# Kernel optimization log

Measured on AMD Instinct MI355X. Metric: run time of the kernel, lower is better.

Reference implementation:

```python
import itertools
import jax, jax.numpy as jnp
import numpy as np

FS = 16000
MAX_TAU = 40
C_SOUND = 343.0
MIC_DISTANCE_FROM_WALL = 0.5
MIN_SPEAKER_HEIGHT = 1.0
MAX_SPEAKER_HEIGHT = 2.0
ROOM = (6.0, 5.0, 3.0)
DENSITY = (0.1, 0.1, 0.1)
N_MICS = 8


def _build_geometry():
    # 8-mic circular array, radius 0.4 m, centered in the room
    ang = np.arange(N_MICS) * 2.0 * np.pi / N_MICS
    receivers = np.stack([3.0 + 0.4 * np.cos(ang),
                          2.5 + 0.4 * np.sin(ang),
                          1.5 * np.ones(N_MICS)], axis=1).astype(np.float32)  # [M,3]
    combinations = np.array(list(itertools.combinations(range(N_MICS), 2)), dtype=np.int32)  # [P,2]
    # candidate grid (same nesting order as the original list comprehension)
    xs = np.arange(MIC_DISTANCE_FROM_WALL, ROOM[0] + DENSITY[0], DENSITY[0], dtype=np.float32)
    ys = np.arange(0.0, ROOM[1] + DENSITY[1], DENSITY[1], dtype=np.float32)
    zs = np.arange(MIN_SPEAKER_HEIGHT, MAX_SPEAKER_HEIGHT + DENSITY[2], DENSITY[2], dtype=np.float32)
    grid_x = np.stack(np.meshgrid(xs, ys, zs, indexing='ij'), axis=-1).reshape(-1, 3)  # [G,3]
    # true TDOA per grid point / pair -> delay index into GCC output of length 2*MAX_TAU+1
    rp = receivers[combinations]                                   # [P,2,3]
    d = np.linalg.norm(grid_x[:, None, None, :] - rp[None], axis=-1)  # [G,P,2]
    tdoa = (d[..., 0] - d[..., 1]) / C_SOUND * FS                  # samples
    tau = np.clip(MAX_TAU + np.round(tdoa), 0, 2 * MAX_TAU).astype(np.int32)  # [G,P]
    rec_centroid = receivers.mean(axis=0)                          # [3]
    return grid_x, tau, combinations, rec_centroid


def setup_inputs() -> dict:
    key = jax.random.key(0)
    signal = jax.random.normal(key, (16, N_MICS, 4096), dtype=jnp.float32)
    grid_x, tau, combinations, rec_centroid = _build_geometry()
    return {
        "signal": signal,
        "grid_x": jnp.asarray(grid_x),
        "tau": jnp.asarray(tau),
        "combinations": jnp.asarray(combinations),
        "rec_centroid": jnp.asarray(rec_centroid),
    }


def reference(signal, grid_x, tau, combinations, rec_centroid):
    B, M, N = signal.shape
    P = combinations.shape[0]
    # GCC-PHAT per mic pair
    pairs = signal[:, combinations, :]                    # [B,P,2,N]
    S = jnp.fft.rfft(pairs, axis=-1)                      # [B,P,2,F]
    X = S[..., 0, :] * jnp.conj(S[..., 1, :])             # cross-spectrum [B,P,F]
    phat = X / (jnp.abs(X) + 1e-12)
    cc = jnp.fft.irfft(phat, n=N, axis=-1)                # [B,P,N]
    # lags -MAX_TAU..MAX_TAU -> length 2*MAX_TAU+1
    cc = jnp.concatenate([cc[..., -MAX_TAU:], cc[..., :MAX_TAU + 1]], axis=-1)  # [B,P,2T+1]
    # gather per grid point / pair (avoids materializing [B,G,P,2T+1])
    gathered = cc[:, jnp.arange(P)[None, :], tau]         # [B,G,P]
    power = gathered.sum(axis=-1)                         # SRP map [B,G]
    idx = jnp.argmax(power, axis=-1)                      # [B]
    x = grid_x[idx]                                       # [B,3]
    return x - rec_centroid
```

## Files before the change

### kernel.cpp

```cpp
#include <hip/hip_runtime.h>

#define N_FFT 4096
#define NH    2048
#define NBINS 2049
#define NLAGS 81
#define MAXTAU 40
#define NSEG  4
#define SEGLEN 512
#define PI_D 3.14159265358979323846

__global__ void table_kernel(double2* __restrict__ tw_fft,
                             double2* __restrict__ tw_post) {
    int idx = blockIdx.x * 256 + (int)threadIdx.x;
    if (idx < 1024) {
        double sv, cv;
        sincos(-(2.0 * PI_D / (double)NH) * (double)idx, &sv, &cv);
        tw_fft[idx] = make_double2(cv, sv);
    } else if (idx < 1024 + NBINS) {
        int k = idx - 1024;
        double sv, cv;
        sincos(-(2.0 * PI_D / (double)N_FFT) * (double)k, &sv, &cv);
        tw_post[k] = make_double2(cv, sv);
    }
}

__global__ __launch_bounds__(1024)
void rfft_kernel(const float* __restrict__ sig,
                 const double2* __restrict__ tw_fft,
                 const double2* __restrict__ tw_post,
                 double* __restrict__ S) {
    int bm  = blockIdx.x;
    int tid = (int)threadIdx.x;

    __shared__ double2 data[NH];

    const float2* sp = (const float2*)(sig + (size_t)bm * N_FFT);
    for (int i = tid; i < NH; i += 1024) {
        float2 v = sp[i];
        int j = (int)(__brev((unsigned)i) >> 21);
        data[j] = make_double2((double)v.x, (double)v.y);
    }
    __syncthreads();

    for (int s = 1; s <= 11; ++s) {
        int half = 1 << (s - 1);
        int t  = tid;
        int g  = t >> (s - 1);
        int j  = t & (half - 1);
        int i0 = (g << s) + j;
        int i1 = i0 + half;
        double2 w = tw_fft[j << (11 - s)];
        double2 u = data[i0];
        double2 v = data[i1];
        double vr = v.x * w.x - v.y * w.y;
        double vi = v.x * w.y + v.y * w.x;
        data[i0] = make_double2(u.x + vr, u.y + vi);
        data[i1] = make_double2(u.x - vr, u.y - vi);
        __syncthreads();
    }

    double* So = S + (size_t)bm * NBINS * 2;
    for (int k = tid; k < NBINS; k += 1024) {
        double2 Zk = data[k & (NH - 1)];
        double2 Zm = data[(NH - k) & (NH - 1)];
        double er = 0.5 * (Zk.x + Zm.x);
        double ei = 0.5 * (Zk.y - Zm.y);
        double dr = Zk.x - Zm.x;
        double di = Zk.y + Zm.y;
        double orr = 0.5 * di;
        double oii = -0.5 * dr;
        double2 w = tw_post[k];
        So[k * 2]     = er + w.x * orr - w.y * oii;
        So[k * 2 + 1] = ei + w.x * oii + w.y * orr;
    }
}

#define NCH 6
#define CHLEN 86
__global__ __launch_bounds__(256)
void phat_cc_part_kernel(const double* __restrict__ S,
                         const int* __restrict__ comb,
                         double* __restrict__ cc_part, int P) {
    int id  = (int)blockIdx.x;
    int seg = id & (NSEG - 1);
    int bp  = id >> 2;
    int b   = bp / P;
    int p   = bp % P;
    int ma = comb[p * 2 + 0];
    int mb = comb[p * 2 + 1];
    const double2* Sa = (const double2*)(S + ((size_t)(b * 8 + ma)) * NBINS * 2);
    const double2* Sb = (const double2*)(S + ((size_t)(b * 8 + mb)) * NBINS * 2);

    int k0 = seg * SEGLEN;
    int k1 = (seg == NSEG - 1) ? NBINS : (k0 + SEGLEN);

    __shared__ double2 phs[SEGLEN + 1];
    __shared__ double partCr[41 * NCH];
    __shared__ double partCi[41 * NCH];

    int tid = (int)threadIdx.x;
    for (int k = k0 + tid; k < k1; k += 256) {
        double2 a = Sa[k];
        double2 c = Sb[k];
        double Xr = a.x * c.x + a.y * c.y;
        double Xi = a.y * c.x - a.x * c.y;
        double mag = sqrt(Xr * Xr + Xi * Xi);
        double w = (k == 0 || k == 2048) ? 1.0 : 2.0;
        double inv = w / (mag + 1e-12);
        phs[k - k0] = make_double2(Xr * inv, Xi * inv);
    }
    __syncthreads();

    if (tid < 41 * NCH) {
        int n = tid % 41;
        int c = tid / 41;
        int kk0 = k0 + c * CHLEN;
        int kk1 = kk0 + CHLEN;
        if (kk1 > k1) kk1 = k1;

        double step = (2.0 * PI_D / (double)N_FFT) * (double)n;
        double sv, cv;
        sincos(step, &sv, &cv);
        double wr = cv, wi = sv;
        sincos(step * (double)kk0, &sv, &cv);
        double rr = cv, ri = sv;

        double Cr = 0.0, Ci = 0.0;
        for (int k = kk0; k < kk1; ++k) {
            double2 ph = phs[k - k0];
            Cr = fma(ph.x, rr, Cr);
            Ci = fma(ph.y, ri, Ci);
            double nr = rr * wr - ri * wi;
            double ni = rr * wi + ri * wr;
            rr = nr; ri = ni;
        }
        partCr[tid] = Cr;
        partCi[tid] = Ci;
    }
    __syncthreads();

    if (tid < 41) {
        double Cr = 0.0, Ci = 0.0;
        #pragma unroll
        for (int c = 0; c < NCH; ++c) {
            Cr += partCr[tid + 41 * c];
            Ci += partCi[tid + 41 * c];
        }
        double* out = cc_part + ((size_t)bp * NSEG + (size_t)seg) * NLAGS;
        out[MAXTAU + tid] = Cr - Ci;
        if (tid > 0) out[MAXTAU - tid] = Cr + Ci;
    }
}

__global__ void cc_reduce_kernel(const double* __restrict__ cc_part,
                                 double* __restrict__ cc, int total) {
    int idx = blockIdx.x * 256 + (int)threadIdx.x;
    if (idx >= total) return;
    int bp  = idx / NLAGS;
    int lag = idx % NLAGS;
    const double* src = cc_part + (size_t)bp * NSEG * NLAGS + lag;
    double v = 0.0;
    #pragma unroll
    for (int s = 0; s < NSEG; ++s) v += src[s * NLAGS];
    cc[idx] = v * (1.0 / (double)N_FFT);
}

__global__ __launch_bounds__(256)
void power_argmax_kernel(const double* __restrict__ cc,
                         const int* __restrict__ tau,
                         int G, int P,
                         double* __restrict__ pval,
                         int* __restrict__ pidx, int nchunks) {
    int b     = (int)blockIdx.y;
    int chunk = (int)blockIdx.x;
    int tid   = (int)threadIdx.x;

    __shared__ double ccs[28 * NLAGS];
    const double2* csrc = (const double2*)(cc + (size_t)b * P * NLAGS);
    double2* cdst = (double2*)ccs;
    for (int i = tid; i < 28 * NLAGS / 2; i += 256) cdst[i] = csrc[i];
    __syncthreads();

    int g = chunk * 256 + tid;
    double v = -1e300;
    int    gi = 0x7fffffff;
    if (g < G) {
        const int4* tp = (const int4*)(tau + (size_t)g * 28);
        v = 0.0;
        #pragma unroll
        for (int q = 0; q < 7; ++q) {
            int4 tv = tp[q];
            v += ccs[(q * 4 + 0) * NLAGS + tv.x];
            v += ccs[(q * 4 + 1) * NLAGS + tv.y];
            v += ccs[(q * 4 + 2) * NLAGS + tv.z];
            v += ccs[(q * 4 + 3) * NLAGS + tv.w];
        }
        gi = g;
    }

    #pragma unroll
    for (int off = 32; off > 0; off >>= 1) {
        double v2 = __shfl_down(v, off);
        int    i2 = __shfl_down(gi, off);
        if (v2 > v || (v2 == v && i2 < gi)) { v = v2; gi = i2; }
    }
    __shared__ double wval[4];
    __shared__ int    widx[4];
    int lane = tid & 63, wv = tid >> 6;
    if (lane == 0) { wval[wv] = v; widx[wv] = gi; }
    __syncthreads();
    if (tid == 0) {
        #pragma unroll
        for (int w = 1; w < 4; ++w) {
            double v2 = wval[w]; int i2 = widx[w];
            if (v2 > v || (v2 == v && i2 < gi)) { v = v2; gi = i2; }
        }
        pval[b * nchunks + chunk] = v;
        pidx[b * nchunks + chunk] = gi;
    }
}

__global__ void finalize_kernel(const double* __restrict__ pval,
                                const int* __restrict__ pidx, int nchunks,
                                const float* __restrict__ grid_x,
                                const float* __restrict__ rec_centroid,
                                float* __restrict__ out) {
    int b = (int)blockIdx.x;
    int l = (int)threadIdx.x;
    double v = -1e300; int gi = 0x7fffffff;
    for (int j = l; j < nchunks; j += 64) {
        double v2 = pval[b * nchunks + j];
        int    i2 = pidx[b * nchunks + j];
        if (v2 > v || (v2 == v && i2 < gi)) { v = v2; gi = i2; }
    }
    #pragma unroll
    for (int off = 32; off > 0; off >>= 1) {
        double v2 = __shfl_down(v, off);
        int    i2 = __shfl_down(gi, off);
        if (v2 > v || (v2 == v && i2 < gi)) { v = v2; gi = i2; }
    }
    if (l == 0) {
        for (int c = 0; c < 3; ++c)
            out[b * 3 + c] = grid_x[(size_t)gi * 3 + c] - rec_centroid[c];
    }
}

extern "C" void kernel_launch(void* const* d_in, const int* in_sizes, int n_in,
                              void* d_out, int out_size, void* d_ws, size_t ws_size,
                              hipStream_t stream) {
    const float* signal       = (const float*)d_in[0];
    const float* grid_x       = (const float*)d_in[1];
    const int*   tau          = (const int*)d_in[2];
    const int*   comb         = (const int*)d_in[3];
    const float* rec_centroid = (const float*)d_in[4];
    float* out = (float*)d_out;

    int G  = in_sizes[1] / 3;
    int P  = in_sizes[3] / 2;
    int BM = in_sizes[0] / N_FFT;
    int B  = BM / 8;
    int BP = B * P;

    double*  S       = (double*)d_ws;
    double*  cc      = S + (size_t)BM * NBINS * 2;
    double*  cc_part = cc + (size_t)BP * NLAGS;
    double2* tw_fft  = (double2*)(cc_part + (size_t)BP * NSEG * NLAGS);
    double2* tw_post = tw_fft + 1024;
    int nchunks = (G + 255) / 256;
    double*  pval = (double*)(tw_post + NBINS);
    int*     pidx = (int*)(pval + (size_t)B * nchunks);

    table_kernel<<<13, 256, 0, stream>>>(tw_fft, tw_post);
    rfft_kernel<<<BM, 1024, 0, stream>>>(signal, tw_fft, tw_post, S);
    phat_cc_part_kernel<<<BP * NSEG, 256, 0, stream>>>(S, comb, cc_part, P);
    cc_reduce_kernel<<<(BP * NLAGS + 255) / 256, 256, 0, stream>>>(cc_part, cc, BP * NLAGS);
    power_argmax_kernel<<<dim3(nchunks, B), 256, 0, stream>>>(cc, tau, G, P, pval, pidx, nchunks);
    finalize_kernel<<<B, 64, 0, stream>>>(pval, pidx, nchunks, grid_x, rec_centroid, out);
}
```

Measured before the change: 109.1 us.

## Fuse cc reduction and finalize into power-argmax, double phat segments

Splits the PHAT/cross-correlation work into 8 segments instead of 4, doubling the number of blocks for more parallelism. The separate cc_reduce kernel is removed: each power_argmax block sums the segment partials itself while loading its shared cc table. The finalize kernel is replaced by a last-block-done ticket scheme using atomics and fences, so the final argmax and output write happen in the last block to finish. Together this removes two kernel launches, at the cost of redundant partial summation in every power block and atomic/fence overhead.

Result: slower. 183.7 us (+68.4%).

```diff
diff --git a/kernel.cpp b/kernel.cpp
--- a/kernel.cpp
+++ b/kernel.cpp
@@ -5,12 +5,13 @@
 #define NBINS 2049
 #define NLAGS 81
 #define MAXTAU 40
-#define NSEG  4
-#define SEGLEN 512
+#define NSEG  8
+#define SEGLEN 256
 #define PI_D 3.14159265358979323846
 
 __global__ void table_kernel(double2* __restrict__ tw_fft,
-                             double2* __restrict__ tw_post) {
+                             double2* __restrict__ tw_post,
+                             int* __restrict__ ticket, int B) {
     int idx = blockIdx.x * 256 + (int)threadIdx.x;
     if (idx < 1024) {
         double sv, cv;
@@ -22,6 +23,7 @@
         sincos(-(2.0 * PI_D / (double)N_FFT) * (double)k, &sv, &cv);
         tw_post[k] = make_double2(cv, sv);
     }
+    if (idx < B) ticket[idx] = 0;
 }
 
 __global__ __launch_bounds__(1024)
@@ -76,14 +78,14 @@
 }
 
 #define NCH 6
-#define CHLEN 86
+#define CHLEN 43
 __global__ __launch_bounds__(256)
 void phat_cc_part_kernel(const double* __restrict__ S,
                          const int* __restrict__ comb,
                          double* __restrict__ cc_part, int P) {
     int id  = (int)blockIdx.x;
     int seg = id & (NSEG - 1);
-    int bp  = id >> 2;
+    int bp  = id >> 3;
     int b   = bp / P;
     int p   = bp % P;
     int ma = comb[p * 2 + 0];
@@ -146,39 +148,36 @@
             Cr += partCr[tid + 41 * c];
             Ci += partCi[tid + 41 * c];
         }
-        double* out = cc_part + ((size_t)bp * NSEG + (size_t)seg) * NLAGS;
-        out[MAXTAU + tid] = Cr - Ci;
-        if (tid > 0) out[MAXTAU - tid] = Cr + Ci;
-    }
-}
-
-__global__ void cc_reduce_kernel(const double* __restrict__ cc_part,
-                                 double* __restrict__ cc, int total) {
-    int idx = blockIdx.x * 256 + (int)threadIdx.x;
-    if (idx >= total) return;
-    int bp  = idx / NLAGS;
-    int lag = idx % NLAGS;
-    const double* src = cc_part + (size_t)bp * NSEG * NLAGS + lag;
-    double v = 0.0;
-    #pragma unroll
-    for (int s = 0; s < NSEG; ++s) v += src[s * NLAGS];
-    cc[idx] = v * (1.0 / (double)N_FFT);
+        double* outp = cc_part + ((size_t)bp * NSEG + (size_t)seg) * NLAGS;
+        outp[MAXTAU + tid] = Cr - Ci;
+        if (tid > 0) outp[MAXTAU - tid] = Cr + Ci;
+    }
 }
 
 __global__ __launch_bounds__(256)
-void power_argmax_kernel(const double* __restrict__ cc,
+void power_argmax_kernel(const double* __restrict__ cc_part,
                          const int* __restrict__ tau,
                          int G, int P,
                          double* __restrict__ pval,
-                         int* __restrict__ pidx, int nchunks) {
+                         int* __restrict__ pidx, int nchunks,
+                         int* __restrict__ ticket,
+                         const float* __restrict__ grid_x,
+                         const float* __restrict__ rec_centroid,
+                         float* __restrict__ out) {
     int b     = (int)blockIdx.y;
     int chunk = (int)blockIdx.x;
     int tid   = (int)threadIdx.x;
 
     __shared__ double ccs[28 * NLAGS];
-    const double2* csrc = (const double2*)(cc + (size_t)b * P * NLAGS);
-    double2* cdst = (double2*)ccs;
-    for (int i = tid; i < 28 * NLAGS / 2; i += 256) cdst[i] = csrc[i];
+    for (int i = tid; i < 28 * NLAGS; i += 256) {
+        int p   = i / NLAGS;
+        int lag = i - p * NLAGS;
+        const double* src = cc_part + ((size_t)(b * P + p) * NSEG) * NLAGS + lag;
+        double v = 0.0;
+        #pragma unroll
+        for (int s = 0; s < NSEG; ++s) v += src[s * NLAGS];
+        ccs[i] = v * (1.0 / (double)N_FFT);
+    }
     __syncthreads();
 
     int g = chunk * 256 + tid;
@@ -206,6 +205,7 @@
     }
     __shared__ double wval[4];
     __shared__ int    widx[4];
+    __shared__ int    lastflag;
     int lane = tid & 63, wv = tid >> 6;
     if (lane == 0) { wval[wv] = v; widx[wv] = gi; }
     __syncthreads();
@@ -215,33 +215,38 @@
             double v2 = wval[w]; int i2 = widx[w];
             if (v2 > v || (v2 == v && i2 < gi)) { v = v2; gi = i2; }
         }
-        pval[b * nchunks + chunk] = v;
-        pidx[b * nchunks + chunk] = gi;
-    }
-}
-
-__global__ void finalize_kernel(const double* __restrict__ pval,
-                                const int* __restrict__ pidx, int nchunks,
-                                const float* __restrict__ grid_x,
-                                const float* __restrict__ rec_centroid,
-                                float* __restrict__ out) {
-    int b = (int)blockIdx.x;
-    int l = (int)threadIdx.x;
-    double v = -1e300; int gi = 0x7fffffff;
-    for (int j = l; j < nchunks; j += 64) {
-        double v2 = pval[b * nchunks + j];
-        int    i2 = pidx[b * nchunks + j];
-        if (v2 > v || (v2 == v && i2 < gi)) { v = v2; gi = i2; }
+        atomicExch(&pval[b * nchunks + chunk], v);
+        atomicExch(&pidx[b * nchunks + chunk], gi);
+        __threadfence();
+        int old = atomicAdd(&ticket[b], 1);
+        lastflag = (old == nchunks - 1) ? 1 : 0;
+    }
+    __syncthreads();
+    if (!lastflag) return;
+
+    __threadfence();
+    double fv = -1e300; int fgi = 0x7fffffff;
+    for (int j = tid; j < nchunks; j += 256) {
+        double v2 = atomicAdd(&pval[b * nchunks + j], 0.0);
+        int    i2 = atomicAdd(&pidx[b * nchunks + j], 0);
+        if (v2 > fv || (v2 == fv && i2 < fgi)) { fv = v2; fgi = i2; }
     }
     #pragma unroll
     for (int off = 32; off > 0; off >>= 1) {
-        double v2 = __shfl_down(v, off);
-        int    i2 = __shfl_down(gi, off);
-        if (v2 > v || (v2 == v && i2 < gi)) { v = v2; gi = i2; }
-    }
-    if (l == 0) {
+        double v2 = __shfl_down(fv, off);
+        int    i2 = __shfl_down(fgi, off);
+        if (v2 > fv || (v2 == fv && i2 < fgi)) { fv = v2; fgi = i2; }
+    }
+    if (lane == 0) { wval[wv] = fv; widx[wv] = fgi; }
+    __syncthreads();
+    if (tid == 0) {
+        #pragma unroll
+        for (int w = 1; w < 4; ++w) {
+            double v2 = wval[w]; int i2 = widx[w];
+            if (v2 > fv || (v2 == fv && i2 < fgi)) { fv = v2; fgi = i2; }
+        }
         for (int c = 0; c < 3; ++c)
-            out[b * 3 + c] = grid_x[(size_t)gi * 3 + c] - rec_centroid[c];
+            out[b * 3 + c] = grid_x[(size_t)fgi * 3 + c] - rec_centroid[c];
     }
 }
 
@@ -262,18 +267,17 @@
     int BP = B * P;
 
     double*  S       = (double*)d_ws;
-    double*  cc      = S + (size_t)BM * NBINS * 2;
-    double*  cc_part = cc + (size_t)BP * NLAGS;
+    double*  cc_part = S + (size_t)BM * NBINS * 2;
     double2* tw_fft  = (double2*)(cc_part + (size_t)BP * NSEG * NLAGS);
     double2* tw_post = tw_fft + 1024;
     int nchunks = (G + 255) / 256;
-    double*  pval = (double*)(tw_post + NBINS);
-    int*     pidx = (int*)(pval + (size_t)B * nchunks);
-
-    table_kernel<<<13, 256, 0, stream>>>(tw_fft, tw_post);
+    double*  pval   = (double*)(tw_post + NBINS);
+    int*     pidx   = (int*)(pval + (size_t)B * nchunks);
+    int*     ticket = pidx + (size_t)B * nchunks;
+
+    table_kernel<<<13, 256, 0, stream>>>(tw_fft, tw_post, ticket, B);
     rfft_kernel<<<BM, 1024, 0, stream>>>(signal, tw_fft, tw_post, S);
     phat_cc_part_kernel<<<BP * NSEG, 256, 0, stream>>>(S, comb, cc_part, P);
-    cc_reduce_kernel<<<(BP * NLAGS + 255) / 256, 256, 0, stream>>>(cc_part, cc, BP * NLAGS);
-    power_argmax_kernel<<<dim3(nchunks, B), 256, 0, stream>>>(cc, tau, G, P, pval, pidx, nchunks);
-    finalize_kernel<<<B, 64, 0, stream>>>(pval, pidx, nchunks, grid_x, rec_centroid, out);
-}
+    power_argmax_kernel<<<dim3(nchunks, B), 256, 0, stream>>>(
+        cc_part, tau, G, P, pval, pidx, nchunks, ticket, grid_x, rec_centroid, out);
+}
```

## Fuse twiddle table and cc reduction into neighbouring kernels via atomics

Applied to the files above, without the earlier changes.

Removes the separate twiddle-table kernel by computing FFT twiddles into shared memory inside the rFFT kernel and computing post-processing twiddles inline with sincos. The partial-cc reduce kernel is also removed: segments now atomically add into a zeroed cc buffer, which the rFFT kernel clears, and the 1/N scale moves into the power kernel's shared-memory load. The segment count doubles to 8 to give the phat kernel more blocks. This cuts two launches and an intermediate buffer, at the cost of fp64 atomics and extra sincos work per FFT block.

Result: no change. 108.3 us (-0.7%).

```diff
diff --git a/kernel.cpp b/kernel.cpp
--- a/kernel.cpp
+++ b/kernel.cpp
@@ -5,34 +5,28 @@
 #define NBINS 2049
 #define NLAGS 81
 #define MAXTAU 40
-#define NSEG  4
-#define SEGLEN 512
+#define NSEG  8
+#define SEGLEN 256
 #define PI_D 3.14159265358979323846
-
-__global__ void table_kernel(double2* __restrict__ tw_fft,
-                             double2* __restrict__ tw_post) {
-    int idx = blockIdx.x * 256 + (int)threadIdx.x;
-    if (idx < 1024) {
-        double sv, cv;
-        sincos(-(2.0 * PI_D / (double)NH) * (double)idx, &sv, &cv);
-        tw_fft[idx] = make_double2(cv, sv);
-    } else if (idx < 1024 + NBINS) {
-        int k = idx - 1024;
-        double sv, cv;
-        sincos(-(2.0 * PI_D / (double)N_FFT) * (double)k, &sv, &cv);
-        tw_post[k] = make_double2(cv, sv);
-    }
-}
 
 __global__ __launch_bounds__(1024)
 void rfft_kernel(const float* __restrict__ sig,
-                 const double2* __restrict__ tw_fft,
-                 const double2* __restrict__ tw_post,
-                 double* __restrict__ S) {
-    int bm  = blockIdx.x;
+                 double* __restrict__ S,
+                 double* __restrict__ cc, int ccN) {
+    int bm  = (int)blockIdx.x;
     int tid = (int)threadIdx.x;
 
     __shared__ double2 data[NH];
+    __shared__ double2 tw[NH / 2];
+
+    for (int i = bm * 1024 + tid; i < ccN; i += (int)gridDim.x * 1024)
+        cc[i] = 0.0;
+
+    {
+        double sv, cv;
+        sincos(-(2.0 * PI_D / (double)NH) * (double)tid, &sv, &cv);
+        tw[tid] = make_double2(cv, sv);
+    }
 
     const float2* sp = (const float2*)(sig + (size_t)bm * N_FFT);
     for (int i = tid; i < NH; i += 1024) {
@@ -44,12 +38,11 @@
 
     for (int s = 1; s <= 11; ++s) {
         int half = 1 << (s - 1);
-        int t  = tid;
-        int g  = t >> (s - 1);
-        int j  = t & (half - 1);
+        int g  = tid >> (s - 1);
+        int j  = tid & (half - 1);
         int i0 = (g << s) + j;
         int i1 = i0 + half;
-        double2 w = tw_fft[j << (11 - s)];
+        double2 w = tw[j << (11 - s)];
         double2 u = data[i0];
         double2 v = data[i1];
         double vr = v.x * w.x - v.y * w.y;
@@ -69,21 +62,22 @@
         double di = Zk.y + Zm.y;
         double orr = 0.5 * di;
         double oii = -0.5 * dr;
-        double2 w = tw_post[k];
-        So[k * 2]     = er + w.x * orr - w.y * oii;
-        So[k * 2 + 1] = ei + w.x * oii + w.y * orr;
+        double sv, cv;
+        sincos(-(2.0 * PI_D / (double)N_FFT) * (double)k, &sv, &cv);
+        So[k * 2]     = er + cv * orr - sv * oii;
+        So[k * 2 + 1] = ei + cv * oii + sv * orr;
     }
 }
 
 #define NCH 6
-#define CHLEN 86
+#define CHLEN 43
 __global__ __launch_bounds__(256)
-void phat_cc_part_kernel(const double* __restrict__ S,
-                         const int* __restrict__ comb,
-                         double* __restrict__ cc_part, int P) {
+void phat_cc_kernel(const double* __restrict__ S,
+                    const int* __restrict__ comb,
+                    double* __restrict__ cc, int P) {
     int id  = (int)blockIdx.x;
     int seg = id & (NSEG - 1);
-    int bp  = id >> 2;
+    int bp  = id >> 3;
     int b   = bp / P;
     int p   = bp % P;
     int ma = comb[p * 2 + 0];
@@ -146,23 +140,10 @@
             Cr += partCr[tid + 41 * c];
             Ci += partCi[tid + 41 * c];
         }
-        double* out = cc_part + ((size_t)bp * NSEG + (size_t)seg) * NLAGS;
-        out[MAXTAU + tid] = Cr - Ci;
-        if (tid > 0) out[MAXTAU - tid] = Cr + Ci;
-    }
-}
-
-__global__ void cc_reduce_kernel(const double* __restrict__ cc_part,
-                                 double* __restrict__ cc, int total) {
-    int idx = blockIdx.x * 256 + (int)threadIdx.x;
-    if (idx >= total) return;
-    int bp  = idx / NLAGS;
-    int lag = idx % NLAGS;
-    const double* src = cc_part + (size_t)bp * NSEG * NLAGS + lag;
-    double v = 0.0;
-    #pragma unroll
-    for (int s = 0; s < NSEG; ++s) v += src[s * NLAGS];
-    cc[idx] = v * (1.0 / (double)N_FFT);
+        double* outp = cc + (size_t)bp * NLAGS;
+        atomicAdd(&outp[MAXTAU + tid], Cr - Ci);
+        if (tid > 0) atomicAdd(&outp[MAXTAU - tid], Cr + Ci);
+    }
 }
 
 __global__ __launch_bounds__(256)
@@ -176,9 +157,9 @@
     int tid   = (int)threadIdx.x;
 
     __shared__ double ccs[28 * NLAGS];
-    const double2* csrc = (const double2*)(cc + (size_t)b * P * NLAGS);
-    double2* cdst = (double2*)ccs;
-    for (int i = tid; i < 28 * NLAGS / 2; i += 256) cdst[i] = csrc[i];
+    const double* csrc = cc + (size_t)b * P * NLAGS;
+    for (int i = tid; i < 28 * NLAGS; i += 256)
+        ccs[i] = csrc[i] * (1.0 / (double)N_FFT);
     __syncthreads();
 
     int g = chunk * 256 + tid;
@@ -261,19 +242,14 @@
     int B  = BM / 8;
     int BP = B * P;
 
-    double*  S       = (double*)d_ws;
-    double*  cc      = S + (size_t)BM * NBINS * 2;
-    double*  cc_part = cc + (size_t)BP * NLAGS;
-    double2* tw_fft  = (double2*)(cc_part + (size_t)BP * NSEG * NLAGS);
-    double2* tw_post = tw_fft + 1024;
+    double* S  = (double*)d_ws;
+    double* cc = S + (size_t)BM * NBINS * 2;
     int nchunks = (G + 255) / 256;
-    double*  pval = (double*)(tw_post + NBINS);
-    int*     pidx = (int*)(pval + (size_t)B * nchunks);
-
-    table_kernel<<<13, 256, 0, stream>>>(tw_fft, tw_post);
-    rfft_kernel<<<BM, 1024, 0, stream>>>(signal, tw_fft, tw_post, S);
-    phat_cc_part_kernel<<<BP * NSEG, 256, 0, stream>>>(S, comb, cc_part, P);
-    cc_reduce_kernel<<<(BP * NLAGS + 255) / 256, 256, 0, stream>>>(cc_part, cc, BP * NLAGS);
+    double* pval = cc + (size_t)BP * NLAGS;
+    int*    pidx = (int*)(pval + (size_t)B * nchunks);
+
+    rfft_kernel<<<BM, 1024, 0, stream>>>(signal, S, cc, BP * NLAGS);
+    phat_cc_kernel<<<BP * NSEG, 256, 0, stream>>>(S, comb, cc, P);
     power_argmax_kernel<<<dim3(nchunks, B), 256, 0, stream>>>(cc, tau, G, P, pval, pidx, nchunks);
     finalize_kernel<<<B, 64, 0, stream>>>(pval, pidx, nchunks, grid_x, rec_centroid, out);
 }
```
